# Performance work log

Measured on AMD Instinct MI355X. Metric: run time of the kernel, lower is better.

The kernel has to match this reference:

```python
import jax, jax.numpy as jnp
import numpy as np
from jax import lax

# ---- quantum-kernel constants: flipped model f = Tr[rho(theta) O(patch)] ----
# rho(theta) = (I + sum_i theta_i P_i)/4 over the 15 non-identity 2-qubit Paulis.
# O(patch)  = (M + M^T)/2 where M is the 3x3 patch zero-padded to 16 and reshaped 4x4.
# Both are linear in their inputs, so precompute A[i,k] = Re Tr[P_i O(e_k)] and
# t0[k] = Tr[O(e_k)] once on the host.

def _pauli_features():
    I = np.eye(2, dtype=np.complex64)
    X = np.array([[0, 1], [1, 0]], np.complex64)
    Y = np.array([[0, -1j], [1j, 0]], np.complex64)
    Z = np.array([[1, 0], [0, -1]], np.complex64)
    singles = [I, X, Y, Z]
    paulis = [np.kron(a, b) for a in singles for b in singles][1:]  # 15 non-identity
    A = np.zeros((15, 9), np.float32)
    t0 = np.zeros((9,), np.float32)
    for k in range(9):
        M = np.zeros((4, 4), np.complex64)
        M.flat[k] = 1.0
        O = (M + M.conj().T) / 2.0
        t0[k] = float(np.real(np.trace(O)))
        for i, P in enumerate(paulis):
            A[i, k] = float(np.real(np.trace(P @ O)))
    return A, t0

_A_NP, _T0_NP = _pauli_features()
STRIDE = 1
PAD = (1, 1)  # (pad_h, pad_w)


def setup_inputs() -> dict:
    key = jax.random.key(0)
    k1, k2, k3 = jax.random.split(key, 3)
    x = jax.random.normal(k1, (32, 16, 128, 128), dtype=jnp.float32)
    weight = jax.random.normal(k2, (64, 16, 15), dtype=jnp.float32)
    bias = jax.random.normal(k3, (64, 1), dtype=jnp.float32)
    return {"x": x, "weight": weight, "bias": bias}


def reference(x, weight, bias):
    B, C, H, W = x.shape
    ph, pw = PAD
    Ho = (H - 3 + 2 * ph) // STRIDE + 1
    Wo = (W - 3 + 2 * pw) // STRIDE + 1
    # im2col: [B, C*9, Ho, Wo], channel-major (C slowest, 3x3 row-major fastest)
    patches = lax.conv_general_dilated_patches(
        x, (3, 3), (STRIDE, STRIDE), ((ph, ph), (pw, pw)))
    patches = patches.reshape(B, C, 9, Ho * Wo)  # [B, C, 9, P]

    A = jnp.asarray(_A_NP)    # [15, 9]
    t0 = jnp.asarray(_T0_NP)  # [9]

    # identity part of rho: sum over in-channels of Tr[O]/4 (weight-independent)
    base = jnp.einsum('k,bckp->bp', t0, patches)            # [B, P]
    # Pauli features Tr[P_i O(patch)] per (channel, patch)
    qf = jnp.einsum('ik,bckp->bcip', A, patches)            # [B, C, 15, P]
    out = (base[:, None, :] + jnp.einsum('oci,bcip->bop', weight, qf)) * 0.25
    out = out + bias                                        # bias [O,1] -> [B,O,P]
    return out.reshape(B, weight.shape[0], Ho, Wo)
```

## Files before the change

### kernel.cpp

```cpp
#include <hip/hip_runtime.h>
#include <hip/hip_bf16.h>


typedef short bf16x8 __attribute__((ext_vector_type(8)));
typedef float f32x4 __attribute__((ext_vector_type(4)));

__device__ __forceinline__ void pauli_entry(int s, int r, int c, float& re, float& im) {
    re = 0.f; im = 0.f;
    if (s == 0)      { if (r == c) re = 1.f; }
    else if (s == 1) { if (r != c) re = 1.f; }
    else if (s == 2) { if (r == 0 && c == 1) im = -1.f; else if (r == 1 && c == 0) im = 1.f; }
    else             { if (r == c) re = (r == 0) ? 1.f : -1.f; }
}

__device__ __forceinline__ float A_entry(int i, int k) {
    int j = i + 1, sa = j >> 2, sb = j & 3;
    int r = k >> 2, c = k & 3;
    float ar, ai, br, bi;
    pauli_entry(sa, r >> 1, c >> 1, ar, ai);
    pauli_entry(sb, r & 1, c & 1, br, bi);
    float re1 = ar * br - ai * bi;
    pauli_entry(sa, c >> 1, r >> 1, ar, ai);
    pauli_entry(sb, c & 1, r & 1, br, bi);
    float re2 = ar * br - ai * bi;
    return 0.5f * (re1 + re2);
}

__device__ __forceinline__ short f2bf(float f) {
    union { float f; unsigned int u; } a; a.f = f;
    unsigned int r = a.u + 0x7fffu + ((a.u >> 16) & 1u);
    return (short)(r >> 16);
}

__device__ __forceinline__ unsigned pk_bf16(float a, float b) {
#if __has_builtin(__builtin_amdgcn_cvt_pk_bf16_f32)
    typedef __bf16 bf2 __attribute__((ext_vector_type(2)));
    bf2 r = __builtin_amdgcn_cvt_pk_bf16_f32(a, b);
    union { bf2 v; unsigned u; } cv; cv.v = r;
    return cv.u;
#else
    union { float f; unsigned u; } x, y; x.f = a; y.f = b;
    unsigned ra = x.u + 0x7fffu + ((x.u >> 16) & 1u);
    unsigned rb = y.u + 0x7fffu + ((y.u >> 16) & 1u);
    return (ra >> 16) | (rb & 0xffff0000u);
#endif
}

__global__ __launch_bounds__(256) void prep_kernel(const float* __restrict__ weight,
                                                   short* __restrict__ bfrag) {
    __shared__ float Ash[135];
    int tid = threadIdx.x;
    if (tid < 135) Ash[tid] = A_entry(tid / 9, tid % 9);
    __syncthreads();

    int t = blockIdx.x * 256 + tid;
    if (t >= 1280) return;
    int lane  = t & 63;
    int ot    = (t >> 6) & 3;
    int chunk = t >> 8;
    int q     = lane >> 4;
    int o     = ot * 16 + (lane & 15);
    short vals[8];
    #pragma unroll
    for (int j = 0; j < 8; ++j) {
        int gk = chunk * 32 + q * 8 + j;
        float v = 0.f;
        if (gk < 144) {
            int tap = gk >> 4;
            int c   = gk & 15;
            float acc = (tap == 0 || tap == 5) ? 1.f : 0.f;
            const float* w = weight + (o * 16 + c) * 15;
            #pragma unroll
            for (int i = 0; i < 15; ++i) acc += w[i] * Ash[i * 9 + tap];
            v = 0.25f * acc;
        }
        vals[j] = f2bf(v);
    }
    *(bf16x8*)(bfrag + t * 8) = *(bf16x8*)vals;
}

__global__ __launch_bounds__(256, 2) void conv_mfma(const float* __restrict__ x,
                                                    const short* __restrict__ bfrag,
                                                    const float* __restrict__ bias,
                                                    float* __restrict__ out) {
    __shared__ short sx[10 * 136 * 16];
    __shared__ __align__(16) float obuf[8192];

    const int tid  = threadIdx.x;
    const int h0   = blockIdx.x * 8;
    const int b    = blockIdx.y;
    const int lane = tid & 63;
    const int wave = tid >> 6;
    const int q    = lane >> 4;
    const int nlo  = lane & 15;

    const float* xb = x + (size_t)b * 16 * 128 * 128;
    #pragma unroll
    for (int it = 0; it < 11; ++it) {
        int pos = tid + it * 256;
        if (pos < 2720) {
            int seg = pos / 136;
            int w   = pos - seg * 136;
            int row = seg >> 1, chalf = seg & 1;
            int hp  = h0 - 1 + row;
            int xw  = w - 4;
            bool ok = ((unsigned)hp < 128u) && ((unsigned)xw < 128u);
            const float* src = xb + (size_t)(chalf * 8) * 16384 + hp * 128 + xw;
            float v[8];
            #pragma unroll
            for (int j = 0; j < 8; ++j)
                v[j] = ok ? src[(size_t)j * 16384] : 0.f;
            int slot = (chalf ^ (w >> 2)) & 1;
            unsigned* dst = (unsigned*)sx + (row * 136 + w) * 8 + slot * 4;
            #pragma unroll
            for (int j2 = 0; j2 < 4; ++j2)
                dst[j2] = pk_bf16(v[2 * j2], v[2 * j2 + 1]);
        }
    }

    bf16x8 Breg[20];
    #pragma unroll
    for (int i = 0; i < 20; ++i)
        Breg[i] = *(const bf16x8*)(bfrag + (i * 64 + lane) * 8);
    float bv[4];
    #pragma unroll
    for (int ot = 0; ot < 4; ++ot) bv[ot] = bias[ot * 16 + nlo];

    int baseA[5];
    #pragma unroll
    for (int ch = 0; ch < 5; ++ch) {
        int tap = ch * 2 + (q >> 1);
        if (tap > 8) tap = 8;
        int kh = tap / 3, kw = tap - 3 * kh;
        int chalf = q & 1;
        int row0  = wave + kh;
        int w0    = nlo + kw + 3;
        int slot  = (chalf ^ (w0 >> 2)) & 1;
        baseA[ch] = (row0 * 136 + w0) * 16 + slot * 8;
    }
    __syncthreads();

    #pragma unroll
    for (int rs = 0; rs < 2; ++rs) {
        f32x4 acc[4][4][2];
        #pragma unroll
        for (int np = 0; np < 4; ++np)
            #pragma unroll
            for (int ot = 0; ot < 4; ++ot) {
                f32x4 ini = { bv[ot], bv[ot], bv[ot], bv[ot] };
                acc[np][ot][0] = ini;
                acc[np][ot][1] = ini;
            }
        #pragma unroll
        for (int np = 0; np < 4; ++np) {
            #pragma unroll
            for (int ch = 0; ch < 5; ++ch) {
                const short* pA = sx + baseA[ch] + rs * 8704 + np * 512;
                bf16x8 A0 = *(const bf16x8*)(pA);
                bf16x8 A1 = *(const bf16x8*)(pA + 256);
                #pragma unroll
                for (int ot = 0; ot < 4; ++ot) {
                    acc[np][ot][0] = __builtin_amdgcn_mfma_f32_16x16x32_bf16(A0, Breg[ch * 4 + ot], acc[np][ot][0], 0, 0, 0);
                    acc[np][ot][1] = __builtin_amdgcn_mfma_f32_16x16x32_bf16(A1, Breg[ch * 4 + ot], acc[np][ot][1], 0, 0, 0);
                }
            }
        }
        #pragma unroll
        for (int ot = 0; ot < 4; ++ot) {
            #pragma unroll
            for (int np = 0; np < 4; ++np)
                #pragma unroll
                for (int mt = 0; mt < 2; ++mt) {
                    int wpart = np * 32 + mt * 16 + q * 4;
                    int widx  = wave * 2048 + nlo * 128 + (wpart ^ ((nlo & 7) << 2));
                    *(f32x4*)(obuf + widx) = acc[np][ot][mt];
                }
            float* outp = out + ((((size_t)b * 64 + ot * 16) * 128)
                                 + h0 + rs * 4 + wave) * 128;
            #pragma unroll
            for (int r = 0; r < 8; ++r) {
                int L  = r * 256 + lane * 4;
                int o  = (L >> 7) & 15;
                int wp = L & 127;
                int ridx = wave * 2048 + o * 128 + (wp ^ ((o & 7) << 2));
                f32x4 v = *(const f32x4*)(obuf + ridx);
                __builtin_nontemporal_store(v, (f32x4*)(outp + (size_t)o * 16384 + wp));
            }
        }
    }
}

extern "C" void kernel_launch(void* const* d_in, const int* in_sizes, int n_in,
                              void* d_out, int out_size, void* d_ws, size_t ws_size,
                              hipStream_t stream) {
    const float* x      = (const float*)d_in[0];
    const float* weight = (const float*)d_in[1];
    const float* bias   = (const float*)d_in[2];
    float* out   = (float*)d_out;
    short* bfrag = (short*)d_ws;

    prep_kernel<<<5, 256, 0, stream>>>(weight, bfrag);
    dim3 grid(16, 32);
    conv_mfma<<<grid, 256, 0, stream>>>(x, bfrag, bias, out);
}
```

Baseline: 196.1 us.

## Split output channels across waves to halve B-fragment registers per wave

Each wave now handles two of the four 16-wide output-channel tiles and four output rows, instead of all four tiles for two rows. This halves the per-wave B-fragment registers and accumulators. The launch-bounds occupancy hint is removed and nontemporal stores are replaced with plain stores. Total MFMA work per block is unchanged, but A-fragment LDS reads are duplicated across the wave pairs that share rows.

```diff
diff --git a/kernel.cpp b/kernel.cpp
--- a/kernel.cpp
+++ b/kernel.cpp
@@ -79,10 +79,10 @@
     *(bf16x8*)(bfrag + t * 8) = *(bf16x8*)vals;
 }
 
-__global__ __launch_bounds__(256, 2) void conv_mfma(const float* __restrict__ x,
-                                                    const short* __restrict__ bfrag,
-                                                    const float* __restrict__ bias,
-                                                    float* __restrict__ out) {
+__global__ __launch_bounds__(256) void conv_mfma(const float* __restrict__ x,
+                                                 const short* __restrict__ bfrag,
+                                                 const float* __restrict__ bias,
+                                                 float* __restrict__ out) {
     __shared__ short sx[10 * 136 * 16];
     __shared__ __align__(16) float obuf[8192];
 
@@ -93,6 +93,8 @@
     const int wave = tid >> 6;
     const int q    = lane >> 4;
     const int nlo  = lane & 15;
+    const int otp  = wave >> 1;
+    const int hh   = wave & 1;
 
     const float* xb = x + (size_t)b * 16 * 128 * 128;
     #pragma unroll
@@ -118,13 +120,15 @@
         }
     }
 
-    bf16x8 Breg[20];
-    #pragma unroll
-    for (int i = 0; i < 20; ++i)
-        Breg[i] = *(const bf16x8*)(bfrag + (i * 64 + lane) * 8);
-    float bv[4];
-    #pragma unroll
-    for (int ot = 0; ot < 4; ++ot) bv[ot] = bias[ot * 16 + nlo];
+    bf16x8 Breg[10];
+    #pragma unroll
+    for (int ch = 0; ch < 5; ++ch)
+        #pragma unroll
+        for (int j = 0; j < 2; ++j)
+            Breg[ch * 2 + j] = *(const bf16x8*)(bfrag + ((ch * 4 + otp * 2 + j) * 64 + lane) * 8);
+    float bv[2];
+    #pragma unroll
+    for (int j = 0; j < 2; ++j) bv[j] = bias[(otp * 2 + j) * 16 + nlo];
 
     int baseA[5];
     #pragma unroll
@@ -133,7 +137,7 @@
         if (tap > 8) tap = 8;
         int kh = tap / 3, kw = tap - 3 * kh;
         int chalf = q & 1;
-        int row0  = wave + kh;
+        int row0  = hh * 4 + kh;
         int w0    = nlo + kw + 3;
         int slot  = (chalf ^ (w0 >> 2)) & 1;
         baseA[ch] = (row0 * 136 + w0) * 16 + slot * 8;
@@ -141,50 +145,49 @@
     __syncthreads();
 
     #pragma unroll
-    for (int rs = 0; rs < 2; ++rs) {
-        f32x4 acc[4][4][2];
-        #pragma unroll
-        for (int np = 0; np < 4; ++np)
-            #pragma unroll
-            for (int ot = 0; ot < 4; ++ot) {
-                f32x4 ini = { bv[ot], bv[ot], bv[ot], bv[ot] };
-                acc[np][ot][0] = ini;
-                acc[np][ot][1] = ini;
+    for (int r = 0; r < 4; ++r) {
+        const int h = h0 + hh * 4 + r;
+        f32x4 acc[2][4][2];
+        #pragma unroll
+        for (int j = 0; j < 2; ++j)
+            #pragma unroll
+            for (int np = 0; np < 4; ++np) {
+                f32x4 ini = { bv[j], bv[j], bv[j], bv[j] };
+                acc[j][np][0] = ini;
+                acc[j][np][1] = ini;
             }
         #pragma unroll
         for (int np = 0; np < 4; ++np) {
             #pragma unroll
             for (int ch = 0; ch < 5; ++ch) {
-                const short* pA = sx + baseA[ch] + rs * 8704 + np * 512;
+                const short* pA = sx + baseA[ch] + r * 2176 + np * 512;
                 bf16x8 A0 = *(const bf16x8*)(pA);
                 bf16x8 A1 = *(const bf16x8*)(pA + 256);
                 #pragma unroll
-                for (int ot = 0; ot < 4; ++ot) {
-                    acc[np][ot][0] = __builtin_amdgcn_mfma_f32_16x16x32_bf16(A0, Breg[ch * 4 + ot], acc[np][ot][0], 0, 0, 0);
-                    acc[np][ot][1] = __builtin_amdgcn_mfma_f32_16x16x32_bf16(A1, Breg[ch * 4 + ot], acc[np][ot][1], 0, 0, 0);
+                for (int j = 0; j < 2; ++j) {
+                    acc[j][np][0] = __builtin_amdgcn_mfma_f32_16x16x32_bf16(A0, Breg[ch * 2 + j], acc[j][np][0], 0, 0, 0);
+                    acc[j][np][1] = __builtin_amdgcn_mfma_f32_16x16x32_bf16(A1, Breg[ch * 2 + j], acc[j][np][1], 0, 0, 0);
                 }
             }
         }
         #pragma unroll
-        for (int ot = 0; ot < 4; ++ot) {
+        for (int j = 0; j < 2; ++j) {
             #pragma unroll
             for (int np = 0; np < 4; ++np)
                 #pragma unroll
                 for (int mt = 0; mt < 2; ++mt) {
-                    int wpart = np * 32 + mt * 16 + q * 4;
-                    int widx  = wave * 2048 + nlo * 128 + (wpart ^ ((nlo & 7) << 2));
-                    *(f32x4*)(obuf + widx) = acc[np][ot][mt];
+                    int px  = np * 32 + mt * 16 + q * 4;
+                    int idx = wave * 2048 + nlo * 128 + (px ^ ((nlo & 7) << 2));
+                    *(f32x4*)(obuf + idx) = acc[j][np][mt];
                 }
-            float* outp = out + ((((size_t)b * 64 + ot * 16) * 128)
-                                 + h0 + rs * 4 + wave) * 128;
-            #pragma unroll
-            for (int r = 0; r < 8; ++r) {
-                int L  = r * 256 + lane * 4;
-                int o  = (L >> 7) & 15;
-                int wp = L & 127;
-                int ridx = wave * 2048 + o * 128 + (wp ^ ((o & 7) << 2));
+            float* outp = out + (((size_t)b * 64 + (otp * 2 + j) * 16) * 128 + h) * 128;
+            #pragma unroll
+            for (int i = 0; i < 8; ++i) {
+                int o   = 2 * i + (lane >> 5);
+                int px  = (lane & 31) * 4;
+                int ridx = wave * 2048 + o * 128 + (px ^ ((o & 7) << 2));
                 f32x4 v = *(const f32x4*)(obuf + ridx);
-                __builtin_nontemporal_store(v, (f32x4*)(outp + (size_t)o * 16384 + wp));
+                *(f32x4*)(outp + (size_t)o * 16384 + px) = v;
             }
         }
     }
```

After: 169.5 us. 1.16x faster.
